# Kernel tuning notes

Hardware: AMD Instinct MI355X
Metric: run time of the kernel (lower is better)

The kernel has to match this reference:

```python
import jax, jax.numpy as jnp
import numpy as np

B, S, H, N, D, R = 2, 2048, 768, 12, 64, 5  # batch, seq, hidden, heads, head_dim, n_structural_deps


def setup_inputs() -> dict:
    key = jax.random.key(0)
    ks = jax.random.split(key, 12)
    hidden_states = jax.random.normal(ks[0], (B, S, H), dtype=jnp.float32)
    attention_mask = jnp.zeros((B, 1, 1, S), dtype=jnp.float32)  # additive mask, all-visible
    # binary structural adjacency per dependency, broadcast over heads
    graph_adj = (jax.random.uniform(ks[1], (R, B, 1, S, S)) < 0.1).astype(jnp.float32)
    s = 0.02
    Wq = jax.random.normal(ks[2], (H, H), dtype=jnp.float32) * s
    bq = jnp.zeros((H,), dtype=jnp.float32)
    Wk = jax.random.normal(ks[3], (H, H), dtype=jnp.float32) * s
    bk = jnp.zeros((H,), dtype=jnp.float32)
    Wv = jax.random.normal(ks[4], (H, H), dtype=jnp.float32) * s
    bv = jnp.zeros((H,), dtype=jnp.float32)
    # biaffine bilinear forms, one [N, D, D] per structural dependency
    bili = jax.random.normal(ks[5], (R, N, D, D), dtype=jnp.float32) * s
    abs_bias = jnp.zeros((R, N), dtype=jnp.float32)  # initialized to zeros as in torch
    return {
        'hidden_states': hidden_states, 'attention_mask': attention_mask,
        'graph_adj': graph_adj, 'Wq': Wq, 'bq': bq, 'Wk': Wk, 'bk': bk,
        'Wv': Wv, 'bv': bv, 'bili': bili, 'abs_bias': abs_bias, 'layer_idx': 0,
    }


def reference(hidden_states, attention_mask, graph_adj, Wq, bq, Wk, bk, Wv, bv,
              bili, abs_bias, layer_idx):
    b, s, h = hidden_states.shape
    n, d = N, D

    def heads(x):  # [b, s, h] -> [b, n, s, d]
        return x.reshape(b, s, n, d).transpose(0, 2, 1, 3)

    q = heads(hidden_states @ Wq.T + bq)
    k = heads(hidden_states @ Wk.T + bk)
    v = heads(hidden_states @ Wv.T + bv)

    scores = jnp.einsum('bnid,bnjd->bnij', q, k)  # [b, n, s, s]
    # biaffine structural bias per dependency, masked by graph adjacency
    for i in range(R):  # small fixed structural loop
        bias = jnp.einsum('bnip,npq,bnjq->bnij', q, bili[i], k)
        bias = bias + abs_bias[i][None, :, None, None]
        scores = scores + bias * graph_adj[i]

    scores = scores / np.sqrt(d).astype(np.float32) + attention_mask
    probs = jax.nn.softmax(scores, axis=-1)
    ctx = jnp.einsum('bnij,bnjd->bnid', probs, v)  # [b, n, s, d]
    return ctx.transpose(0, 2, 1, 3).reshape(b, s, h)
```

## Files before the change

kernel.cpp:

```cpp
#include <hip/hip_runtime.h>
#include <cstdint>
#include <cstddef>

#define B_  2
#define S_  2048
#define H_  768
#define NH  12
#define DH  64
#define RD  5
#define BN  (B_*NH)

typedef _Float16 f16;
typedef __attribute__((ext_vector_type(8))) _Float16 f16x8;
typedef __attribute__((ext_vector_type(4))) float f32x4;

#define MFMA16(a, b, c) __builtin_amdgcn_mfma_f32_16x16x32_f16((a), (b), (c), 0, 0, 0)

#if __has_builtin(__builtin_amdgcn_exp2f)
__device__ __forceinline__ float exp2fast(float x) { return __builtin_amdgcn_exp2f(x); }
#else
__device__ __forceinline__ float exp2fast(float x) { return __expf(0.69314718056f * x); }
#endif

#define SCL 0.1803368801f
#define L2E 1.44269504f

#define NX4 ((B_*S_*H_)/4)
#define NW4 ((H_*H_)/4)

__global__ __launch_bounds__(256) void cvtall(
    const float* __restrict__ x,
    const float* __restrict__ wq, const float* __restrict__ wk,
    const float* __restrict__ wv,
    f16* __restrict__ xh, f16* __restrict__ wh)
{
    int idx = blockIdx.x * 256 + threadIdx.x;
    const int total4 = NX4 + 3 * NW4;
    if (idx >= total4) return;
    const float* src;
    f16* dst;
    int off;
    if (idx < NX4) {
        src = x; dst = xh; off = idx;
    } else {
        int r = idx - NX4;
        int which = r / NW4;
        off = r - which * NW4;
        src = (which == 0) ? wq : (which == 1) ? wk : wv;
        dst = wh + (size_t)which * H_ * H_;
    }
    float4 f = ((const float4*)src)[off];
    f16 h[4] = {(f16)f.x, (f16)f.y, (f16)f.z, (f16)f.w};
    ((ushort4*)dst)[off] = *(const ushort4*)h;
}

__global__ __launch_bounds__(256, 3) void qkv_gemm(
    const f16* __restrict__ xh, const f16* __restrict__ wh,
    const float* __restrict__ bq, const float* __restrict__ bk,
    const float* __restrict__ bv,
    f16* __restrict__ qo, f16* __restrict__ ko, f16* __restrict__ vt)
{
    __shared__ __align__(16) f16 Xs[64][72];
    __shared__ __align__(16) f16 Ws[3][64][72];

    const int tid = threadIdx.x;
    const int n  = blockIdx.x;
    const int m0 = blockIdx.y * 64;
    const int w = tid >> 6, lane = tid & 63;
    const int l15 = lane & 15, quad = lane >> 4;
    const int srow = tid >> 2, sc0 = (tid & 3) * 16;

    f32x4 acc[3][4];
#pragma unroll
    for (int i = 0; i < 3; ++i)
#pragma unroll
        for (int ns = 0; ns < 4; ++ns) acc[i][ns] = (f32x4){0.f, 0.f, 0.f, 0.f};

    const f16* xsrc = xh + (size_t)(m0 + srow) * H_ + sc0;
    const f16* wsrc = wh + (size_t)(n * 64 + srow) * H_ + sc0;

    for (int kc = 0; kc < 12; ++kc) {
        __syncthreads();
        {
            const f16* s0 = xsrc + kc * 64;
            *(f16x8*)&Xs[srow][sc0]     = *(const f16x8*)(s0);
            *(f16x8*)&Xs[srow][sc0 + 8] = *(const f16x8*)(s0 + 8);
        }
#pragma unroll
        for (int i = 0; i < 3; ++i) {
            const f16* s0 = wsrc + (size_t)i * H_ * H_ + kc * 64;
            *(f16x8*)&Ws[i][srow][sc0]     = *(const f16x8*)(s0);
            *(f16x8*)&Ws[i][srow][sc0 + 8] = *(const f16x8*)(s0 + 8);
        }
        __syncthreads();

        f16x8 a0 = *(const f16x8*)&Xs[w * 16 + l15][quad * 8];
        f16x8 a1 = *(const f16x8*)&Xs[w * 16 + l15][quad * 8 + 32];
#pragma unroll
        for (int i = 0; i < 3; ++i)
#pragma unroll
            for (int ns = 0; ns < 4; ++ns) {
                f16x8 b0 = *(const f16x8*)&Ws[i][ns * 16 + l15][quad * 8];
                f16x8 b1 = *(const f16x8*)&Ws[i][ns * 16 + l15][quad * 8 + 32];
                acc[i][ns] = MFMA16(a0, b0, acc[i][ns]);
                acc[i][ns] = MFMA16(a1, b1, acc[i][ns]);
            }
    }
    __syncthreads();

    const float* bias[3] = {bq, bk, bv};
    f16 (*T0)[72] = Xs;
    f16 (*T1)[72] = Ws[0];
    f16 (*T2)[72] = Ws[1];
#pragma unroll
    for (int i = 0; i < 3; ++i) {
        f16 (*T)[72] = (i == 0) ? T0 : (i == 1) ? T1 : T2;
#pragma unroll
        for (int ns = 0; ns < 4; ++ns) {
            float bb = bias[i][n * 64 + ns * 16 + l15];
#pragma unroll
            for (int reg = 0; reg < 4; ++reg)
                T[w * 16 + quad * 4 + reg][ns * 16 + l15] =
                    (f16)(acc[i][ns][reg] + bb);
        }
    }
    __syncthreads();

    const int mrow = m0 + srow;
    const int bb2 = mrow >> 11, ss = mrow & 2047;
    {
        f16* dst = qo + ((size_t)(bb2 * NH + n) * S_ + ss) * DH + sc0;
        *(f16x8*)dst       = *(const f16x8*)&T0[srow][sc0];
        *(f16x8*)(dst + 8) = *(const f16x8*)&T0[srow][sc0 + 8];
    }
    {
        f16* dst = ko + ((size_t)(bb2 * NH + n) * S_ + ss) * DH + sc0;
        *(f16x8*)dst       = *(const f16x8*)&T1[srow][sc0];
        *(f16x8*)(dst + 8) = *(const f16x8*)&T1[srow][sc0 + 8];
    }
    {
        f16 tmp[16];
#pragma unroll
        for (int u = 0; u < 16; ++u) tmp[u] = T2[sc0 + u][srow];
        f16* dst = vt + ((size_t)(bb2 * NH + n) * DH + srow) * S_ + (m0 & 2047) + sc0;
        *(f16x8*)dst       = *(const f16x8*)&tmp[0];
        *(f16x8*)(dst + 8) = *(const f16x8*)&tmp[8];
    }
}

__global__ __launch_bounds__(256) void adjpack(
    const float* __restrict__ adj, unsigned char* __restrict__ adjp)
{
    const int idx = blockIdx.x * 256 + threadIdx.x;
    const int j  = idx & 2047;
    const int iq = (idx >> 11) & 511;
    const int b  = idx >> 20;
    unsigned int bits[4] = {0, 0, 0, 0};
#pragma unroll
    for (int r = 0; r < RD; ++r) {
#pragma unroll
        for (int ii = 0; ii < 4; ++ii) {
            float a = adj[(((size_t)(r * B_ + b) * S_) + iq * 4 + ii) * S_ + j];
            bits[ii] |= (a != 0.f ? 1u : 0u) << r;
        }
    }
    uchar4 pk;
    pk.x = (unsigned char)bits[0];
    pk.y = (unsigned char)bits[1];
    pk.z = (unsigned char)bits[2];
    pk.w = (unsigned char)bits[3];
    *(uchar4*)(adjp + (size_t)idx * 4) = pk;
}

__global__ __launch_bounds__(256, 3) void attn(
    const f16* __restrict__ q, const f16* __restrict__ k, const f16* __restrict__ vt,
    const float* __restrict__ bili, const unsigned char* __restrict__ adjp,
    const float* __restrict__ mask, const float* __restrict__ absb,
    float* __restrict__ out)
{
    __shared__ __align__(16) char smem[9216 + 9216 + 128];
    f16*   Mt  = (f16*)smem;
    f16*   Pb  = (f16*)(smem + 9216);
    float* lut = (float*)(smem + 9216 + 9216);

    const int tid = threadIdx.x;
    const int idx = blockIdx.x;
    const int g = idx & 7;
    const int it = (idx >> 3) & 31;
    const int bn = 8 * (idx >> 8) + g;
    const int b = bn / NH, n = bn % NH;
    const int w = tid >> 6, lane = tid & 63;
    const int l15 = lane & 15, quad = lane >> 4;
    const int wi0 = it * 64 + w * 16;
    const size_t kbase = (size_t)bn * S_ * DH;

    if (tid < 32) {
        float a = 0.f;
#pragma unroll
        for (int r = 0; r < RD; ++r)
            if (tid & (1 << r)) a += absb[r * NH + n];
        lut[tid] = a * SCL;
    }

    const f16* qrow = q + kbase + (size_t)(wi0 + l15) * DH + quad * 8;
    f16x8 aq0 = *(const f16x8*)(qrow);
    f16x8 aq1 = *(const f16x8*)(qrow + 32);

    f16* Pw = Pb + w * 16 * 72;

    f16x8 aqp[RD][2];
#pragma unroll 1
    for (int r = 0; r < RD; ++r) {
        __syncthreads();
        {
            int p = tid >> 2, q0 = (tid & 3) * 16;
            const float* src = bili + ((size_t)(r * NH + n) * DH + p) * DH + q0;
            float4 g0 = ((const float4*)src)[0];
            float4 g1 = ((const float4*)src)[1];
            float4 g2 = ((const float4*)src)[2];
            float4 g3 = ((const float4*)src)[3];
            float mv[16] = {g0.x, g0.y, g0.z, g0.w, g1.x, g1.y, g1.z, g1.w,
                            g2.x, g2.y, g2.z, g2.w, g3.x, g3.y, g3.z, g3.w};
#pragma unroll
            for (int u = 0; u < 16; ++u) Mt[(q0 + u) * 72 + p] = (f16)mv[u];
        }
        __syncthreads();
#pragma unroll
        for (int ns = 0; ns < 4; ++ns) {
            f16x8 b0 = *(const f16x8*)&Mt[(ns * 16 + l15) * 72 + quad * 8];
            f16x8 b1 = *(const f16x8*)&Mt[(ns * 16 + l15) * 72 + quad * 8 + 32];
            f32x4 d = {0.f, 0.f, 0.f, 0.f};
            d = MFMA16(aq0, b0, d);
            d = MFMA16(aq1, b1, d);
#pragma unroll
            for (int reg = 0; reg < 4; ++reg)
                Pw[(quad * 4 + reg) * 72 + ns * 16 + l15] = (f16)d[reg];
        }
        aqp[r][0] = *(const f16x8*)&Pw[l15 * 72 + quad * 8];
        aqp[r][1] = *(const f16x8*)&Pw[l15 * 72 + quad * 8 + 32];
    }

    f16x8 ones;
#pragma unroll
    for (int u = 0; u < 8; ++u) ones[u] = (f16)1.0f;

    f32x4 o[4] = {{0,0,0,0},{0,0,0,0},{0,0,0,0},{0,0,0,0}};
    f32x4 lacc = {0.f, 0.f, 0.f, 0.f};
    float mrun[4] = {-1e30f, -1e30f, -1e30f, -1e30f};

    const unsigned char* adjrow =
        adjp + (size_t)(b * 512 + (wi0 >> 2) + quad) * (S_ * 4);
    const float* maskrow = mask + (size_t)b * S_;
    const f16* vtb = vt + (size_t)bn * DH * S_;

    for (int t = 0; t < 32; ++t) {
        const int j0 = t * 64;
        float sc[4][4];

#pragma unroll
        for (int js = 0; js < 4; ++js) {
            const int jcol = j0 + js * 16 + l15;
            const f16* kp = k + kbase + (size_t)jcol * DH + quad * 8;
            f16x8 bk0 = *(const f16x8*)(kp);
            f16x8 bk1 = *(const f16x8*)(kp + 32);

            f32x4 aqk = {0.f, 0.f, 0.f, 0.f};
            aqk = MFMA16(aq0, bk0, aqk);
            aqk = MFMA16(aq1, bk1, aqk);
            f32x4 ar[RD];
#pragma unroll
            for (int r = 0; r < RD; ++r) {
                f32x4 z = {0.f, 0.f, 0.f, 0.f};
                z = MFMA16(aqp[r][0], bk0, z);
                z = MFMA16(aqp[r][1], bk1, z);
                ar[r] = z;
            }

            uchar4 a4 = *(const uchar4*)(adjrow + (size_t)jcol * 4);
            unsigned int bbits[4] = {a4.x, a4.y, a4.z, a4.w};
            float mkL = maskrow[jcol] * L2E;
#pragma unroll
            for (int reg = 0; reg < 4; ++reg) {
                float s = aqk[reg];
                unsigned int bt = bbits[reg];
#pragma unroll
                for (int r = 0; r < RD; ++r)
                    s = fmaf((float)((bt >> r) & 1u), ar[r][reg], s);
                sc[js][reg] = fmaf(s, SCL, lut[bt] + mkL);
            }
        }

        float alpha[4];
#pragma unroll
        for (int reg = 0; reg < 4; ++reg) {
            float nm = fmaxf(fmaxf(sc[0][reg], sc[1][reg]),
                             fmaxf(sc[2][reg], sc[3][reg]));
#pragma unroll
            for (int off = 1; off < 16; off <<= 1)
                nm = fmaxf(nm, __shfl_xor(nm, off));
            float mn = fmaxf(mrun[reg], nm);
            alpha[reg] = exp2fast(mrun[reg] - mn);
            mrun[reg] = mn;
        }
#pragma unroll
        for (int js = 0; js < 4; ++js)
#pragma unroll
            for (int reg = 0; reg < 4; ++reg) {
                float p = exp2fast(sc[js][reg] - mrun[reg]);
                Pw[(quad * 4 + reg) * 72 + js * 16 + l15] = (f16)p;
            }
#pragma unroll
        for (int reg = 0; reg < 4; ++reg) {
            lacc[reg] *= alpha[reg];
#pragma unroll
            for (int ds = 0; ds < 4; ++ds) o[ds][reg] *= alpha[reg];
        }

        f16x8 pa0 = *(const f16x8*)&Pw[l15 * 72 + quad * 8];
        f16x8 pa1 = *(const f16x8*)&Pw[l15 * 72 + quad * 8 + 32];
        lacc = MFMA16(pa0, ones, lacc);
        lacc = MFMA16(pa1, ones, lacc);
#pragma unroll
        for (int ds = 0; ds < 4; ++ds) {
            const f16* vp = vtb + (size_t)(ds * 16 + l15) * S_ + j0 + quad * 8;
            f16x8 bv0 = *(const f16x8*)(vp);
            f16x8 bv1 = *(const f16x8*)(vp + 32);
            o[ds] = MFMA16(pa0, bv0, o[ds]);
            o[ds] = MFMA16(pa1, bv1, o[ds]);
        }
    }

#pragma unroll
    for (int reg = 0; reg < 4; ++reg) {
        float inv = 1.f / lacc[reg];
        int i = wi0 + quad * 4 + reg;
#pragma unroll
        for (int ds = 0; ds < 4; ++ds)
            out[((size_t)b * S_ + i) * H_ + n * DH + ds * 16 + l15] =
                o[ds][reg] * inv;
    }
}

extern "C" void kernel_launch(void* const* d_in, const int* in_sizes, int n_in,
                              void* d_out, int out_size, void* d_ws, size_t ws_size,
                              hipStream_t stream)
{
    const float* hs   = (const float*)d_in[0];
    const float* mask = (const float*)d_in[1];
    const float* adj  = (const float*)d_in[2];
    const float* Wq   = (const float*)d_in[3];
    const float* bq   = (const float*)d_in[4];
    const float* Wk   = (const float*)d_in[5];
    const float* bk   = (const float*)d_in[6];
    const float* Wv   = (const float*)d_in[7];
    const float* bv   = (const float*)d_in[8];
    const float* bili = (const float*)d_in[9];
    const float* absb = (const float*)d_in[10];
    float* out = (float*)d_out;

    const size_t QKV = (size_t)BN * S_ * DH;
    f16* q  = (f16*)d_ws;
    f16* k  = q + QKV;
    f16* vt = k + QKV;
    unsigned char* adjp = (unsigned char*)(vt + QKV);
    f16* xh = (f16*)(adjp + (size_t)B_ * 512 * S_ * 4);
    f16* wh = xh + (size_t)B_ * S_ * H_;

    const int total4 = NX4 + 3 * NW4;
    cvtall<<<(total4 + 255) / 256, 256, 0, stream>>>(hs, Wq, Wk, Wv, xh, wh);
    qkv_gemm<<<dim3(12, 64), 256, 0, stream>>>(xh, wh, bq, bk, bv, q, k, vt);
    adjpack<<<8192, 256, 0, stream>>>(adj, adjp);
    attn<<<768, 256, 0, stream>>>(q, k, vt, bili, adjp, mask, absb, out);
}
```

Measured before the change: 520.9 us.

## Stage K and V tiles through LDS with double-buffered async global_load_lds

Instead of each wave reading K and V^T directly from global memory for every 64-column tile, the block cooperatively loads K and V tiles into double-buffered shared memory with direct global-to-LDS loads, prefetching the next tile while computing the current one. The P and bilinear scratch buffers use an XOR swizzle instead of padding, so bank-conflict-free reads fit in the new layout. The absolute-bias lookup table is replaced by per-register adds of the bias inside the masked FMA. This cuts redundant global traffic across the four waves at the cost of a block-wide barrier per tile and more shared memory, which may lower occupancy.

```diff
diff --git a/kernel.cpp b/kernel.cpp
--- a/kernel.cpp
+++ b/kernel.cpp
@@ -27,6 +27,11 @@
 
 #define NX4 ((B_*S_*H_)/4)
 #define NW4 ((H_*H_)/4)
+
+typedef __attribute__((address_space(3))) void       lds_vp;
+typedef __attribute__((address_space(1))) const void glb_vp;
+#define GLDS16(src, dst) \
+    __builtin_amdgcn_global_load_lds((glb_vp*)(src), (lds_vp*)(dst), 16, 0, 0)
 
 __global__ __launch_bounds__(256) void cvtall(
     const float* __restrict__ x,
@@ -178,10 +183,9 @@
     const float* __restrict__ mask, const float* __restrict__ absb,
     float* __restrict__ out)
 {
-    __shared__ __align__(16) char smem[9216 + 9216 + 128];
-    f16*   Mt  = (f16*)smem;
-    f16*   Pb  = (f16*)(smem + 9216);
-    float* lut = (float*)(smem + 9216 + 9216);
+    __shared__ __align__(16) f16 Kb[2][4096];
+    __shared__ __align__(16) f16 Vb[2][4096];
+    __shared__ __align__(16) f16 Pb[4][1024];
 
     const int tid = threadIdx.x;
     const int idx = blockIdx.x;
@@ -194,19 +198,14 @@
     const int wi0 = it * 64 + w * 16;
     const size_t kbase = (size_t)bn * S_ * DH;
 
-    if (tid < 32) {
-        float a = 0.f;
-#pragma unroll
-        for (int r = 0; r < RD; ++r)
-            if (tid & (1 << r)) a += absb[r * NH + n];
-        lut[tid] = a * SCL;
-    }
-
     const f16* qrow = q + kbase + (size_t)(wi0 + l15) * DH + quad * 8;
     f16x8 aq0 = *(const f16x8*)(qrow);
     f16x8 aq1 = *(const f16x8*)(qrow + 32);
 
-    f16* Pw = Pb + w * 16 * 72;
+    f16* Pw = &Pb[w][0];
+    f16* Mt = &Kb[0][0];
+    const int pswz0 = ((quad ^ (l15 & 7)) << 3);
+    const int pswz1 = (((quad + 4) ^ (l15 & 7)) << 3);
 
     f16x8 aqp[RD][2];
 #pragma unroll 1
@@ -232,13 +231,38 @@
             f32x4 d = {0.f, 0.f, 0.f, 0.f};
             d = MFMA16(aq0, b0, d);
             d = MFMA16(aq1, b1, d);
-#pragma unroll
-            for (int reg = 0; reg < 4; ++reg)
-                Pw[(quad * 4 + reg) * 72 + ns * 16 + l15] = (f16)d[reg];
-        }
-        aqp[r][0] = *(const f16x8*)&Pw[l15 * 72 + quad * 8];
-        aqp[r][1] = *(const f16x8*)&Pw[l15 * 72 + quad * 8 + 32];
-    }
+            const int cb = ns * 2 + (l15 >> 3);
+#pragma unroll
+            for (int reg = 0; reg < 4; ++reg) {
+                const int row = quad * 4 + reg;
+                Pw[row * 64 + ((cb ^ (row & 7)) << 3) + (l15 & 7)] = (f16)d[reg];
+            }
+        }
+        aqp[r][0] = *(const f16x8*)&Pw[l15 * 64 + pswz0];
+        aqp[r][1] = *(const f16x8*)&Pw[l15 * 64 + pswz1];
+    }
+    __syncthreads();
+
+    const f16* kg  = k + kbase;
+    const f16* vtb = vt + (size_t)bn * DH * S_;
+    const int rsub = lane >> 3;
+    const int csw8 = (((lane & 7) ^ (rsub & 7)) << 3);
+
+    auto stage = [&](int buf, int jt0) {
+#pragma unroll
+        for (int ii = 0; ii < 2; ++ii) {
+            const int inst = w * 2 + ii;
+            const int row = inst * 8 + rsub;
+            GLDS16(kg + (size_t)(jt0 + row) * DH + csw8, &Kb[buf][inst * 512]);
+            GLDS16(vtb + (size_t)row * S_ + jt0 + csw8, &Vb[buf][inst * 512]);
+        }
+    };
+
+    stage(0, 0);
+
+    float ab[RD];
+#pragma unroll
+    for (int r = 0; r < RD; ++r) ab[r] = absb[r * NH + n];
 
     f16x8 ones;
 #pragma unroll
@@ -251,18 +275,20 @@
     const unsigned char* adjrow =
         adjp + (size_t)(b * 512 + (wi0 >> 2) + quad) * (S_ * 4);
     const float* maskrow = mask + (size_t)b * S_;
-    const f16* vtb = vt + (size_t)bn * DH * S_;
 
     for (int t = 0; t < 32; ++t) {
+        __syncthreads();
+        if (t < 31) stage((t + 1) & 1, (t + 1) * 64);
+        const f16* KT = &Kb[t & 1][0];
+        const f16* VT = &Vb[t & 1][0];
         const int j0 = t * 64;
         float sc[4][4];
 
 #pragma unroll
         for (int js = 0; js < 4; ++js) {
-            const int jcol = j0 + js * 16 + l15;
-            const f16* kp = k + kbase + (size_t)jcol * DH + quad * 8;
-            f16x8 bk0 = *(const f16x8*)(kp);
-            f16x8 bk1 = *(const f16x8*)(kp + 32);
+            const int jrow = js * 16 + l15;
+            f16x8 bk0 = *(const f16x8*)&KT[jrow * 64 + pswz0];
+            f16x8 bk1 = *(const f16x8*)&KT[jrow * 64 + pswz1];
 
             f32x4 aqk = {0.f, 0.f, 0.f, 0.f};
             aqk = MFMA16(aq0, bk0, aqk);
@@ -276,6 +302,7 @@
                 ar[r] = z;
             }
 
+            const int jcol = j0 + jrow;
             uchar4 a4 = *(const uchar4*)(adjrow + (size_t)jcol * 4);
             unsigned int bbits[4] = {a4.x, a4.y, a4.z, a4.w};
             float mkL = maskrow[jcol] * L2E;
@@ -285,8 +312,8 @@
                 unsigned int bt = bbits[reg];
 #pragma unroll
                 for (int r = 0; r < RD; ++r)
-                    s = fmaf((float)((bt >> r) & 1u), ar[r][reg], s);
-                sc[js][reg] = fmaf(s, SCL, lut[bt] + mkL);
+                    s = fmaf((float)((bt >> r) & 1u), ar[r][reg] + ab[r], s);
+                sc[js][reg] = fmaf(s, SCL, mkL);
             }
         }
 
@@ -303,12 +330,15 @@
             mrun[reg] = mn;
         }
 #pragma unroll
-        for (int js = 0; js < 4; ++js)
+        for (int js = 0; js < 4; ++js) {
+            const int cb = js * 2 + (l15 >> 3);
 #pragma unroll
             for (int reg = 0; reg < 4; ++reg) {
+                const int row = quad * 4 + reg;
                 float p = exp2fast(sc[js][reg] - mrun[reg]);
-                Pw[(quad * 4 + reg) * 72 + js * 16 + l15] = (f16)p;
+                Pw[row * 64 + ((cb ^ (row & 7)) << 3) + (l15 & 7)] = (f16)p;
             }
+        }
 #pragma unroll
         for (int reg = 0; reg < 4; ++reg) {
             lacc[reg] *= alpha[reg];
@@ -316,15 +346,15 @@
             for (int ds = 0; ds < 4; ++ds) o[ds][reg] *= alpha[reg];
         }
 
-        f16x8 pa0 = *(const f16x8*)&Pw[l15 * 72 + quad * 8];
-        f16x8 pa1 = *(const f16x8*)&Pw[l15 * 72 + quad * 8 + 32];
+        f16x8 pa0 = *(const f16x8*)&Pw[l15 * 64 + pswz0];
+        f16x8 pa1 = *(const f16x8*)&Pw[l15 * 64 + pswz1];
         lacc = MFMA16(pa0, ones, lacc);
         lacc = MFMA16(pa1, ones, lacc);
 #pragma unroll
         for (int ds = 0; ds < 4; ++ds) {
-            const f16* vp = vtb + (size_t)(ds * 16 + l15) * S_ + j0 + quad * 8;
-            f16x8 bv0 = *(const f16x8*)(vp);
-            f16x8 bv1 = *(const f16x8*)(vp + 32);
+            const int vrow = ds * 16 + l15;
+            f16x8 bv0 = *(const f16x8*)&VT[vrow * 64 + pswz0];
+            f16x8 bv1 = *(const f16x8*)&VT[vrow * 64 + pswz1];
             o[ds] = MFMA16(pa0, bv0, o[ds]);
             o[ds] = MFMA16(pa1, bv1, o[ds]);
         }
```

After: 532.4 us. +2.2%, slower.
